# Kernel tuning notes

Measured on AMD Instinct MI355X. Metric: run time of the kernel, lower is better.

Reference implementation:

```python
import math
import jax, jax.numpy as jnp
import numpy as np

N_GAUSS = 1_000_000
EPS = 1e-8


def setup_inputs() -> dict:
    key = jax.random.key(0)
    k1, k2, k3 = jax.random.split(key, 3)
    init_extent = 50.0
    means = (jax.random.uniform(k1, (N_GAUSS, 3), dtype=jnp.float32) - 0.5) * 2.0 * init_extent
    log_scales = jnp.full((N_GAUSS, 3), math.log(0.05), dtype=jnp.float32)
    quats = jax.random.normal(k2, (N_GAUSS, 4), dtype=jnp.float32)
    sh_coeffs = jax.random.normal(k3, (N_GAUSS, 16, 3), dtype=jnp.float32) * 0.01
    opa_logit = math.log(0.1 / 0.9)  # inverse_sigmoid(init_opacity=0.1)
    opacity_camera = jnp.full((N_GAUSS, 1), opa_logit, dtype=jnp.float32)
    opacity_lidar = jnp.full((N_GAUSS, 1), opa_logit, dtype=jnp.float32)
    camera_to_world = jnp.eye(4, dtype=jnp.float32)
    lidar_to_world = jnp.eye(4, dtype=jnp.float32)
    intrinsics = jnp.array([[1000.0, 0.0, 800.0], [0.0, 1000.0, 450.0], [0.0, 0.0, 1.0]], dtype=jnp.float32)
    return dict(means=means, log_scales=log_scales, quats=quats, sh_coeffs=sh_coeffs,
                opacity_camera=opacity_camera, opacity_lidar=opacity_lidar,
                camera_to_world=camera_to_world, intrinsics=intrinsics,
                lidar_to_world=lidar_to_world,
                rgb_width=1600, rgb_height=900, lidar_width=1024, lidar_height=128,
                fov_min_deg=-25, fov_max_deg=3, near_plane=1, far_plane=100)


def _bilinear_scatter(u, v, w, vals, H, W, wrap_u):
    """Scatter vals [N,C] with weights w [N] at continuous pixel coords (u,v)
    using bilinear splatting. Returns [H, W, C+1] (weighted vals, weight sum)."""
    u0 = jnp.floor(u)
    v0 = jnp.floor(v)
    fu = u - u0
    fv = v - v0
    u0i = u0.astype(jnp.int32)
    v0i = v0.astype(jnp.int32)
    acc = jnp.zeros((H * W, vals.shape[-1] + 1), dtype=vals.dtype)
    corners = ((0, 0, (1.0 - fu) * (1.0 - fv)), (1, 0, fu * (1.0 - fv)),
               (0, 1, (1.0 - fu) * fv), (1, 1, fu * fv))
    for du, dv, cw in corners:
        ui = u0i + du
        vi = v0i + dv
        if wrap_u:
            ui = jnp.mod(ui, W)
            ok_u = jnp.ones_like(ui, dtype=bool)
        else:
            ok_u = (ui >= 0) & (ui < W)
        ok = ok_u & (vi >= 0) & (vi < H)
        ww = w * cw * ok.astype(w.dtype)
        idx = jnp.clip(vi, 0, H - 1) * W + jnp.clip(ui, 0, W - 1)
        payload = jnp.concatenate([vals * ww[:, None], ww[:, None]], axis=-1)
        acc = acc.at[idx].add(payload)
    return acc.reshape(H, W, -1)


def reference(means, log_scales, quats, sh_coeffs, opacity_camera, opacity_lidar,
              camera_to_world, intrinsics, lidar_to_world,
              rgb_width, rgb_height, lidar_width, lidar_height,
              fov_min_deg, fov_max_deg, near_plane, far_plane):
    H, W = int(rgb_height), int(rgb_width)
    HL, WL = int(lidar_height), int(lidar_width)
    near = float(near_plane)
    far = float(far_plane)

    # ---- camera (point-splat proxy of gsplat rasterization) ----
    w2c = jnp.linalg.inv(camera_to_world)
    pts_c = means @ w2c[:3, :3].T + w2c[:3, 3]  # [N,3] camera frame
    x, y, z = pts_c[:, 0], pts_c[:, 1], pts_c[:, 2]
    valid_c = (z > near) & (z < far)
    zs = jnp.where(valid_c, z, 1.0)
    u = intrinsics[0, 0] * x / zs + intrinsics[0, 2]
    v = intrinsics[1, 1] * y / zs + intrinsics[1, 2]
    opa_c = jax.nn.sigmoid(jnp.clip(opacity_camera[:, 0], -20.0, 20.0))
    colors = jax.nn.sigmoid(sh_coeffs[:, 0, :])  # DC band, as in render_rgb
    wc = opa_c * valid_c.astype(opa_c.dtype)
    vals_c = jnp.concatenate([colors, z[:, None]], axis=-1)  # [N,4] (rgb, depth)
    acc = _bilinear_scatter(u, v, wc, vals_c, H, W, wrap_u=False)
    wsum = acc[..., 4]
    alpha = jnp.clip(wsum, 0.0, 1.0)
    rgb = acc[..., :3] / (wsum[..., None] + EPS) * alpha[..., None]  # black background
    depth = acc[..., 3] / (wsum + EPS)

    # ---- LiDAR (custom spherical bilinear range-image splat, mean aggregation) ----
    w2l = jnp.linalg.inv(lidar_to_world)
    pts_l = means @ w2l[:3, :3].T + w2l[:3, 3]
    r = jnp.linalg.norm(pts_l, axis=-1)
    az = jnp.arctan2(pts_l[:, 1], pts_l[:, 0])
    el = jnp.arcsin(pts_l[:, 2] / jnp.maximum(r, 1e-6))
    fmin = math.radians(float(fov_min_deg))
    fmax = math.radians(float(fov_max_deg))
    uL = (az / (2.0 * jnp.pi) + 0.5) * WL          # azimuth wraps around
    vL = (fmax - el) / (fmax - fmin) * (HL - 1)    # elevation row
    valid_l = (r > near) & (r < far) & (el >= fmin) & (el <= fmax)
    opa_l = jax.nn.sigmoid(jnp.clip(opacity_lidar[:, 0], -20.0, 20.0))
    wl = opa_l * valid_l.astype(opa_l.dtype)
    acc_l = _bilinear_scatter(uL, vL, wl, r[:, None], HL, WL, wrap_u=True)
    lw = acc_l[..., 1]
    lidar_depth = acc_l[..., 0] / (lw + EPS)  # 'mean' depth aggregation
    lidar_alpha = jnp.clip(lw, 0.0, 1.0)

    return (rgb, depth, alpha, lidar_depth, lidar_alpha)
```

## Files before the change

kernel.cpp:

```cpp
#include <hip/hip_runtime.h>
#include <math.h>

#define EPSV 1e-8f
#define PI_D 3.14159265358979323846
#define NREP 8

__device__ float g_mats[32];

__device__ __forceinline__ void invert4x4_reg(const float* __restrict__ m,
                                              float* __restrict__ out) {
    double a00=m[0], a01=m[1], a02=m[2], a03=m[3];
    double a10=m[4], a11=m[5], a12=m[6], a13=m[7];
    double a20=m[8], a21=m[9], a22=m[10],a23=m[11];
    double a30=m[12],a31=m[13],a32=m[14],a33=m[15];

    double b00 = a00*a11 - a01*a10;
    double b01 = a00*a12 - a02*a10;
    double b02 = a00*a13 - a03*a10;
    double b03 = a01*a12 - a02*a11;
    double b04 = a01*a13 - a03*a11;
    double b05 = a02*a13 - a03*a12;
    double b06 = a20*a31 - a21*a30;
    double b07 = a20*a32 - a22*a30;
    double b08 = a20*a33 - a23*a30;
    double b09 = a21*a32 - a22*a31;
    double b10 = a21*a33 - a23*a31;
    double b11 = a22*a33 - a23*a32;

    double det = b00*b11 - b01*b10 + b02*b09 + b03*b08 - b04*b07 + b05*b06;
    double inv = 1.0 / det;

    out[0]  = (float)(( a11*b11 - a12*b10 + a13*b09) * inv);
    out[1]  = (float)((-a01*b11 + a02*b10 - a03*b09) * inv);
    out[2]  = (float)(( a31*b05 - a32*b04 + a33*b03) * inv);
    out[3]  = (float)((-a21*b05 + a22*b04 - a23*b03) * inv);
    out[4]  = (float)((-a10*b11 + a12*b08 - a13*b07) * inv);
    out[5]  = (float)(( a00*b11 - a02*b08 + a03*b07) * inv);
    out[6]  = (float)((-a30*b05 + a32*b02 - a33*b01) * inv);
    out[7]  = (float)(( a20*b05 - a22*b02 + a23*b01) * inv);
    out[8]  = (float)(( a10*b10 - a11*b08 + a13*b06) * inv);
    out[9]  = (float)((-a00*b10 + a01*b08 - a03*b06) * inv);
    out[10] = (float)(( a30*b04 - a31*b02 + a33*b00) * inv);
    out[11] = (float)((-a20*b04 + a21*b02 - a23*b00) * inv);
    out[12] = (float)((-a10*b09 + a11*b07 - a12*b06) * inv);
    out[13] = (float)(( a00*b09 - a01*b07 + a02*b06) * inv);
    out[14] = (float)((-a30*b03 + a31*b01 - a32*b00) * inv);
    out[15] = (float)(( a20*b03 - a21*b01 + a22*b00) * inv);
}

__global__ void prep_kernel(const float* __restrict__ c2w,
                            const float* __restrict__ l2w) {
    if (blockIdx.x == 0 && threadIdx.x == 0) {
        invert4x4_reg(c2w, g_mats);
        invert4x4_reg(l2w, g_mats + 16);
    }
}

__device__ __forceinline__ float sigmoid_clipped(float x) {
    #pragma clang fp contract(off)
    x = fminf(fmaxf(x, -20.0f), 20.0f);
    return 1.0f / (1.0f + expf(-x));
}

__global__ __launch_bounds__(256) void scatter_cam(
    const float* __restrict__ means,
    const float* __restrict__ sh,
    const float* __restrict__ opa_c,
    const float* __restrict__ intr,
    float* __restrict__ acc,
    const int* __restrict__ p_W, const int* __restrict__ p_H,
    const int* __restrict__ p_near, const int* __restrict__ p_far,
    int N)
{
    #pragma clang fp contract(off)
    const int t = blockIdx.x * blockDim.x + threadIdx.x;
    if (t >= N) return;

    const int W = *p_W, H = *p_H;
    const float nearp = (float)(*p_near);
    const float farp  = (float)(*p_far);
    const long long HW = (long long)W * H;

    float* C  = acc;
    float* Wp = acc + 4 * HW;

    const float fx = intr[0], cx = intr[2], fy = intr[4], cy = intr[5];
    const float* w2c = g_mats;

    const float px = means[3 * t + 0];
    const float py = means[3 * t + 1];
    const float pz = means[3 * t + 2];

    float x = w2c[0] * px + w2c[1] * py + w2c[2]  * pz + w2c[3];
    float y = w2c[4] * px + w2c[5] * py + w2c[6]  * pz + w2c[7];
    float z = w2c[8] * px + w2c[9] * py + w2c[10] * pz + w2c[11];
    if (!(z > nearp && z < farp)) return;

    float u = fx * x / z + cx;
    float v = fy * y / z + cy;
    float wc = sigmoid_clipped(opa_c[t]);
    const float* shp = sh + 48LL * t;
    float c0 = 1.0f / (1.0f + expf(-shp[0]));
    float c1 = 1.0f / (1.0f + expf(-shp[1]));
    float c2 = 1.0f / (1.0f + expf(-shp[2]));

    float u0f = floorf(u), v0f = floorf(v);
    float fu = u - u0f, fv = v - v0f;
    int u0 = (int)u0f, v0 = (int)v0f;
    #pragma unroll
    for (int c = 0; c < 4; c++) {
        int du = c & 1, dv = c >> 1;
        int ui = u0 + du, vi = v0 + dv;
        if (ui >= 0 && ui < W && vi >= 0 && vi < H) {
            float cw = (du ? fu : 1.0f - fu) * (dv ? fv : 1.0f - fv);
            float ww = wc * cw;
            long long idx = (long long)vi * W + ui;
            float* g = C + idx * 4;
            atomicAdd(g + 0, c0 * ww);
            atomicAdd(g + 1, c1 * ww);
            atomicAdd(g + 2, c2 * ww);
            atomicAdd(g + 3, z * ww);
            atomicAdd(Wp + idx, ww);
        }
    }
}

__global__ __launch_bounds__(256) void scatter_lid(
    const float* __restrict__ means,
    const float* __restrict__ opa_l,
    float* __restrict__ acc,
    const int* __restrict__ p_W, const int* __restrict__ p_H,
    const int* __restrict__ p_WL, const int* __restrict__ p_HL,
    const int* __restrict__ p_fmin, const int* __restrict__ p_fmax,
    const int* __restrict__ p_near, const int* __restrict__ p_far,
    int N)
{
    #pragma clang fp contract(off)
    const int t = blockIdx.x * blockDim.x + threadIdx.x;
    if (t >= N) return;

    const int W = *p_W, H = *p_H, WL = *p_WL, HL = *p_HL;
    const float nearp = (float)(*p_near);
    const float farp  = (float)(*p_far);
    const double dfmin = (double)(*p_fmin) * PI_D / 180.0;
    const double dfmax = (double)(*p_fmax) * PI_D / 180.0;
    const float ffmin  = (float)dfmin;
    const float ffmax  = (float)dfmax;
    const float denomL = (float)(dfmax - dfmin);
    const float twopi  = (float)(2.0 * PI_D);

    const long long HW  = (long long)W * H;
    const long long LHW = (long long)WL * HL;

    float* Lr = acc + 5 * HW + (long long)(blockIdx.x & (NREP - 1)) * 2 * LHW;

    const float* w2l = g_mats + 16;

    const float px = means[3 * t + 0];
    const float py = means[3 * t + 1];
    const float pz = means[3 * t + 2];

    float x = w2l[0] * px + w2l[1] * py + w2l[2]  * pz + w2l[3];
    float y = w2l[4] * px + w2l[5] * py + w2l[6]  * pz + w2l[7];
    float z = w2l[8] * px + w2l[9] * py + w2l[10] * pz + w2l[11];
    float rr = ((x * x) + (y * y)) + (z * z);
    float r = sqrtf(rr);
    float q  = z / fmaxf(r, 1e-6f);
    float el = (float)asin((double)q);
    if (!(r > nearp && r < farp && el >= ffmin && el <= ffmax)) return;

    float az = (float)atan2((double)y, (double)x);
    float uL = (az / twopi + 0.5f) * (float)WL;
    float vL = (ffmax - el) / denomL * (float)(HL - 1);
    float wl = sigmoid_clipped(opa_l[t]);

    float u0f = floorf(uL), v0f = floorf(vL);
    float fu = uL - u0f, fv = vL - v0f;
    int u0 = (int)u0f, v0 = (int)v0f;
    #pragma unroll
    for (int c = 0; c < 4; c++) {
        int du = c & 1, dv = c >> 1;
        int ui = u0 + du, vi = v0 + dv;
        if (ui >= WL) ui -= WL;
        if (vi >= 0 && vi < HL) {
            float cw = (du ? fu : 1.0f - fu) * (dv ? fv : 1.0f - fv);
            float ww = wl * cw;
            long long idx = (long long)vi * WL + ui;
            atomicAdd(Lr + 2 * idx + 0, r * ww);
            atomicAdd(Lr + 2 * idx + 1, ww);
        }
    }
}

__global__ __launch_bounds__(256) void finalize_acc(
    const float* __restrict__ acc,
    float* __restrict__ out,
    const int* __restrict__ p_W, const int* __restrict__ p_H,
    const int* __restrict__ p_WL, const int* __restrict__ p_HL)
{
    const int W = *p_W, H = *p_H, WL = *p_WL, HL = *p_HL;
    const long long HW = (long long)W * H;
    const long long LHW = (long long)WL * HL;
    const long long depthOff = 3 * HW;
    const long long alphaOff = 4 * HW;
    const long long ldOff    = 5 * HW;
    const long long laOff    = 5 * HW + LHW;

    const float* C  = acc;
    const float* Wp = acc + 4 * HW;
    const float* L  = acc + 5 * HW;

    long long i = (long long)blockIdx.x * blockDim.x + threadIdx.x;
    if (i < HW) {
        float4 p = *reinterpret_cast<const float4*>(C + 4 * i);
        float wsum = Wp[i];
        float a = fminf(fmaxf(wsum, 0.0f), 1.0f);
        float inv = 1.0f / (wsum + EPSV);
        float s = inv * a;
        out[3 * i + 0] = p.x * s;
        out[3 * i + 1] = p.y * s;
        out[3 * i + 2] = p.z * s;
        out[depthOff + i] = p.w * inv;
        out[alphaOff + i] = a;
    }
    if (i < LHW) {
        float ld = 0.0f, lw = 0.0f;
        #pragma unroll
        for (int k = 0; k < NREP; k++) {
            float2 l = *reinterpret_cast<const float2*>(L + (long long)k * 2 * LHW + 2 * i);
            ld += l.x;
            lw += l.y;
        }
        out[ldOff + i] = ld * (1.0f / (lw + EPSV));
        out[laOff + i] = fminf(fmaxf(lw, 0.0f), 1.0f);
    }
}

__global__ __launch_bounds__(256) void scatter_fb(
    const float* __restrict__ means,
    const float* __restrict__ sh,
    const float* __restrict__ opa_c,
    const float* __restrict__ opa_l,
    const float* __restrict__ intr,
    const int* __restrict__ p_W, const int* __restrict__ p_H,
    const int* __restrict__ p_WL, const int* __restrict__ p_HL,
    const int* __restrict__ p_fmin, const int* __restrict__ p_fmax,
    const int* __restrict__ p_near, const int* __restrict__ p_far,
    float* __restrict__ out, int N)
{
    #pragma clang fp contract(off)
    const int t = blockIdx.x * blockDim.x + threadIdx.x;
    if (t >= N) return;

    const int W = *p_W, H = *p_H, WL = *p_WL, HL = *p_HL;
    const float nearp = (float)(*p_near);
    const float farp  = (float)(*p_far);
    const double dfmin = (double)(*p_fmin) * PI_D / 180.0;
    const double dfmax = (double)(*p_fmax) * PI_D / 180.0;
    const float ffmin  = (float)dfmin;
    const float ffmax  = (float)dfmax;
    const float denomL = (float)(dfmax - dfmin);
    const float twopi  = (float)(2.0 * PI_D);

    const long long HW = (long long)W * H;
    const long long LHW = (long long)WL * HL;
    const long long depthOff = 3 * HW;
    const long long alphaOff = 4 * HW;
    const long long ldOff    = 5 * HW;
    const long long laOff    = 5 * HW + LHW;

    const float fx = intr[0], cx = intr[2], fy = intr[4], cy = intr[5];
    const float* w2c = g_mats;
    const float* w2l = g_mats + 16;

    const float px = means[3 * t + 0];
    const float py = means[3 * t + 1];
    const float pz = means[3 * t + 2];
    {
        float x = w2c[0] * px + w2c[1] * py + w2c[2]  * pz + w2c[3];
        float y = w2c[4] * px + w2c[5] * py + w2c[6]  * pz + w2c[7];
        float z = w2c[8] * px + w2c[9] * py + w2c[10] * pz + w2c[11];
        if (z > nearp && z < farp) {
            float u = fx * x / z + cx;
            float v = fy * y / z + cy;
            float wc = sigmoid_clipped(opa_c[t]);
            const float* shp = sh + 48LL * t;
            float c0 = 1.0f / (1.0f + expf(-shp[0]));
            float c1 = 1.0f / (1.0f + expf(-shp[1]));
            float c2 = 1.0f / (1.0f + expf(-shp[2]));

            float u0f = floorf(u), v0f = floorf(v);
            float fu = u - u0f, fv = v - v0f;
            int u0 = (int)u0f, v0 = (int)v0f;
            #pragma unroll
            for (int c = 0; c < 4; c++) {
                int du = c & 1, dv = c >> 1;
                int ui = u0 + du, vi = v0 + dv;
                if (ui >= 0 && ui < W && vi >= 0 && vi < H) {
                    float cw = (du ? fu : 1.0f - fu) * (dv ? fv : 1.0f - fv);
                    float ww = wc * cw;
                    long long idx = (long long)vi * W + ui;
                    atomicAdd(&out[idx * 3 + 0], c0 * ww);
                    atomicAdd(&out[idx * 3 + 1], c1 * ww);
                    atomicAdd(&out[idx * 3 + 2], c2 * ww);
                    atomicAdd(&out[depthOff + idx], z * ww);
                    atomicAdd(&out[alphaOff + idx], ww);
                }
            }
        }
    }
    {
        float x = w2l[0] * px + w2l[1] * py + w2l[2]  * pz + w2l[3];
        float y = w2l[4] * px + w2l[5] * py + w2l[6]  * pz + w2l[7];
        float z = w2l[8] * px + w2l[9] * py + w2l[10] * pz + w2l[11];
        float rr = ((x * x) + (y * y)) + (z * z);
        float r = sqrtf(rr);
        float q  = z / fmaxf(r, 1e-6f);
        float el = (float)asin((double)q);
        if (r > nearp && r < farp && el >= ffmin && el <= ffmax) {
            float az = (float)atan2((double)y, (double)x);
            float uL = (az / twopi + 0.5f) * (float)WL;
            float vL = (ffmax - el) / denomL * (float)(HL - 1);
            float wl = sigmoid_clipped(opa_l[t]);

            float u0f = floorf(uL), v0f = floorf(vL);
            float fu = uL - u0f, fv = vL - v0f;
            int u0 = (int)u0f, v0 = (int)v0f;
            #pragma unroll
            for (int c = 0; c < 4; c++) {
                int du = c & 1, dv = c >> 1;
                int ui = u0 + du, vi = v0 + dv;
                if (ui >= WL) ui -= WL;
                if (vi >= 0 && vi < HL) {
                    float cw = (du ? fu : 1.0f - fu) * (dv ? fv : 1.0f - fv);
                    float ww = wl * cw;
                    long long idx = (long long)vi * WL + ui;
                    atomicAdd(&out[ldOff + idx], r * ww);
                    atomicAdd(&out[laOff + idx], ww);
                }
            }
        }
    }
}

__global__ __launch_bounds__(256) void finalize_fb(
    float* __restrict__ out,
    const int* __restrict__ p_W, const int* __restrict__ p_H,
    const int* __restrict__ p_WL, const int* __restrict__ p_HL)
{
    const int W = *p_W, H = *p_H, WL = *p_WL, HL = *p_HL;
    const long long HW = (long long)W * H;
    const long long LHW = (long long)WL * HL;
    const long long depthOff = 3 * HW;
    const long long alphaOff = 4 * HW;
    const long long ldOff    = 5 * HW;
    const long long laOff    = 5 * HW + LHW;

    long long i = (long long)blockIdx.x * blockDim.x + threadIdx.x;
    if (i < HW) {
        float wsum = out[alphaOff + i];
        float a = fminf(fmaxf(wsum, 0.0f), 1.0f);
        float inv = 1.0f / (wsum + EPSV);
        float s = inv * a;
        out[3 * i + 0] *= s;
        out[3 * i + 1] *= s;
        out[3 * i + 2] *= s;
        out[depthOff + i] *= inv;
        out[alphaOff + i] = a;
    }
    if (i < LHW) {
        float wsum = out[laOff + i];
        out[ldOff + i] *= 1.0f / (wsum + EPSV);
        out[laOff + i] = fminf(fmaxf(wsum, 0.0f), 1.0f);
    }
}

extern "C" void kernel_launch(void* const* d_in, const int* in_sizes, int n_in,
                              void* d_out, int out_size, void* d_ws, size_t ws_size,
                              hipStream_t stream) {
    const float* means  = (const float*)d_in[0];
    const float* sh     = (const float*)d_in[3];
    const float* opa_c  = (const float*)d_in[4];
    const float* opa_l  = (const float*)d_in[5];
    const float* c2w    = (const float*)d_in[6];
    const float* intr   = (const float*)d_in[7];
    const float* l2w    = (const float*)d_in[8];
    const int* p_W    = (const int*)d_in[9];
    const int* p_H    = (const int*)d_in[10];
    const int* p_WL   = (const int*)d_in[11];
    const int* p_HL   = (const int*)d_in[12];
    const int* p_fmin = (const int*)d_in[13];
    const int* p_fmax = (const int*)d_in[14];
    const int* p_near = (const int*)d_in[15];
    const int* p_far  = (const int*)d_in[16];

    const int N = in_sizes[0] / 3;
    float* out = (float*)d_out;
    float* acc = (float*)d_ws;

    const long long HW  = 1600LL * 900LL;
    const long long LHW = 1024LL * 128LL;
    const size_t need_bytes =
        (5 * (size_t)HW + (size_t)NREP * 2 * (size_t)LHW) * sizeof(float);

    const int sgrid = (N + 255) / 256;
    const int fgrid = (int)((HW + 255) / 256);

    prep_kernel<<<1, 64, 0, stream>>>(c2w, l2w);

    if (ws_size >= need_bytes) {
        hipMemsetAsync(d_ws, 0, need_bytes, stream);
        scatter_cam<<<sgrid, 256, 0, stream>>>(
            means, sh, opa_c, intr, acc,
            p_W, p_H, p_near, p_far, N);
        scatter_lid<<<sgrid, 256, 0, stream>>>(
            means, opa_l, acc,
            p_W, p_H, p_WL, p_HL, p_fmin, p_fmax, p_near, p_far, N);
        finalize_acc<<<fgrid, 256, 0, stream>>>(
            acc, out, p_W, p_H, p_WL, p_HL);
    } else {
        hipMemsetAsync(d_out, 0, (size_t)out_size * sizeof(float), stream);
        scatter_fb<<<sgrid, 256, 0, stream>>>(
            means, sh, opa_c, opa_l, intr,
            p_W, p_H, p_WL, p_HL, p_fmin, p_fmax, p_near, p_far,
            out, N);
        finalize_fb<<<fgrid, 256, 0, stream>>>(
            out, p_W, p_H, p_WL, p_HL);
    }
}
```

Measured before the change: 426.3 us.

## Fuse camera and lidar scatters with packed 64-bit CAS accumulation

Merges the camera and lidar scatter kernels into one kernel and drops the separate matrix-inversion kernel. Each block now inverts the 4x4 matrices into shared memory. Pairs of float accumulators are packed into 64-bit words and updated with a compare-and-swap loop, which cuts the number of atomic operations per corner. The cost is possible CAS retry loops under contention, since many Gaussians hit the same pixels, plus redundant per-block matrix inversion in double precision.

```diff
diff --git a/kernel.cpp b/kernel.cpp
--- a/kernel.cpp
+++ b/kernel.cpp
@@ -5,7 +5,7 @@
 #define PI_D 3.14159265358979323846
 #define NREP 8
 
-__device__ float g_mats[32];
+typedef unsigned long long ull_t;
 
 __device__ __forceinline__ void invert4x4_reg(const float* __restrict__ m,
                                               float* __restrict__ out) {
@@ -48,86 +48,35 @@
     out[15] = (float)(( a20*b03 - a21*b01 + a22*b00) * inv);
 }
 
-__global__ void prep_kernel(const float* __restrict__ c2w,
-                            const float* __restrict__ l2w) {
-    if (blockIdx.x == 0 && threadIdx.x == 0) {
-        invert4x4_reg(c2w, g_mats);
-        invert4x4_reg(l2w, g_mats + 16);
-    }
-}
-
 __device__ __forceinline__ float sigmoid_clipped(float x) {
     #pragma clang fp contract(off)
     x = fminf(fmaxf(x, -20.0f), 20.0f);
     return 1.0f / (1.0f + expf(-x));
 }
 
-__global__ __launch_bounds__(256) void scatter_cam(
+__device__ __forceinline__ ull_t pack2(float a, float b) {
+    return ((ull_t)__float_as_uint(b) << 32) | (ull_t)__float_as_uint(a);
+}
+__device__ __forceinline__ void cas_add2(ull_t* p, float da, float db) {
+    ull_t old = *p;
+    while (true) {
+        float a = __uint_as_float((unsigned int)(old & 0xffffffffULL));
+        float b = __uint_as_float((unsigned int)(old >> 32));
+        ull_t desired = pack2(a + da, b + db);
+        ull_t got = atomicCAS(p, old, desired);
+        if (got == old) break;
+        old = got;
+    }
+}
+
+__global__ __launch_bounds__(256) void scatter_pk(
     const float* __restrict__ means,
     const float* __restrict__ sh,
     const float* __restrict__ opa_c,
+    const float* __restrict__ opa_l,
     const float* __restrict__ intr,
-    float* __restrict__ acc,
-    const int* __restrict__ p_W, const int* __restrict__ p_H,
-    const int* __restrict__ p_near, const int* __restrict__ p_far,
-    int N)
-{
-    #pragma clang fp contract(off)
-    const int t = blockIdx.x * blockDim.x + threadIdx.x;
-    if (t >= N) return;
-
-    const int W = *p_W, H = *p_H;
-    const float nearp = (float)(*p_near);
-    const float farp  = (float)(*p_far);
-    const long long HW = (long long)W * H;
-
-    float* C  = acc;
-    float* Wp = acc + 4 * HW;
-
-    const float fx = intr[0], cx = intr[2], fy = intr[4], cy = intr[5];
-    const float* w2c = g_mats;
-
-    const float px = means[3 * t + 0];
-    const float py = means[3 * t + 1];
-    const float pz = means[3 * t + 2];
-
-    float x = w2c[0] * px + w2c[1] * py + w2c[2]  * pz + w2c[3];
-    float y = w2c[4] * px + w2c[5] * py + w2c[6]  * pz + w2c[7];
-    float z = w2c[8] * px + w2c[9] * py + w2c[10] * pz + w2c[11];
-    if (!(z > nearp && z < farp)) return;
-
-    float u = fx * x / z + cx;
-    float v = fy * y / z + cy;
-    float wc = sigmoid_clipped(opa_c[t]);
-    const float* shp = sh + 48LL * t;
-    float c0 = 1.0f / (1.0f + expf(-shp[0]));
-    float c1 = 1.0f / (1.0f + expf(-shp[1]));
-    float c2 = 1.0f / (1.0f + expf(-shp[2]));
-
-    float u0f = floorf(u), v0f = floorf(v);
-    float fu = u - u0f, fv = v - v0f;
-    int u0 = (int)u0f, v0 = (int)v0f;
-    #pragma unroll
-    for (int c = 0; c < 4; c++) {
-        int du = c & 1, dv = c >> 1;
-        int ui = u0 + du, vi = v0 + dv;
-        if (ui >= 0 && ui < W && vi >= 0 && vi < H) {
-            float cw = (du ? fu : 1.0f - fu) * (dv ? fv : 1.0f - fv);
-            float ww = wc * cw;
-            long long idx = (long long)vi * W + ui;
-            float* g = C + idx * 4;
-            atomicAdd(g + 0, c0 * ww);
-            atomicAdd(g + 1, c1 * ww);
-            atomicAdd(g + 2, c2 * ww);
-            atomicAdd(g + 3, z * ww);
-            atomicAdd(Wp + idx, ww);
-        }
-    }
-}
-
-__global__ __launch_bounds__(256) void scatter_lid(
-    const float* __restrict__ means,
-    const float* __restrict__ opa_l,
+    const float* __restrict__ c2w,
+    const float* __restrict__ l2w,
     float* __restrict__ acc,
     const int* __restrict__ p_W, const int* __restrict__ p_H,
     const int* __restrict__ p_WL, const int* __restrict__ p_HL,
@@ -136,6 +85,13 @@
     int N)
 {
     #pragma clang fp contract(off)
+    __shared__ float sm[32];
+    if (threadIdx.x == 0) {
+        invert4x4_reg(c2w, sm);
+        invert4x4_reg(l2w, sm + 16);
+    }
+    __syncthreads();
+
     const int t = blockIdx.x * blockDim.x + threadIdx.x;
     if (t >= N) return;
 
@@ -152,47 +108,85 @@
     const long long HW  = (long long)W * H;
     const long long LHW = (long long)WL * HL;
 
-    float* Lr = acc + 5 * HW + (long long)(blockIdx.x & (NREP - 1)) * 2 * LHW;
-
-    const float* w2l = g_mats + 16;
+    ull_t* C01 = (ull_t*)acc;
+    ull_t* C23 = (ull_t*)(acc + 2 * HW);
+    float* Wp  = acc + 4 * HW;
+    ull_t* Lr  = (ull_t*)(acc + 5 * HW) + (long long)(blockIdx.x & (NREP - 1)) * LHW;
+
+    const float fx = intr[0], cx = intr[2], fy = intr[4], cy = intr[5];
+    const float* w2c = sm;
+    const float* w2l = sm + 16;
 
     const float px = means[3 * t + 0];
     const float py = means[3 * t + 1];
     const float pz = means[3 * t + 2];
 
-    float x = w2l[0] * px + w2l[1] * py + w2l[2]  * pz + w2l[3];
-    float y = w2l[4] * px + w2l[5] * py + w2l[6]  * pz + w2l[7];
-    float z = w2l[8] * px + w2l[9] * py + w2l[10] * pz + w2l[11];
-    float rr = ((x * x) + (y * y)) + (z * z);
-    float r = sqrtf(rr);
-    float q  = z / fmaxf(r, 1e-6f);
-    float el = (float)asin((double)q);
-    if (!(r > nearp && r < farp && el >= ffmin && el <= ffmax)) return;
-
-    float az = (float)atan2((double)y, (double)x);
-    float uL = (az / twopi + 0.5f) * (float)WL;
-    float vL = (ffmax - el) / denomL * (float)(HL - 1);
-    float wl = sigmoid_clipped(opa_l[t]);
-
-    float u0f = floorf(uL), v0f = floorf(vL);
-    float fu = uL - u0f, fv = vL - v0f;
-    int u0 = (int)u0f, v0 = (int)v0f;
-    #pragma unroll
-    for (int c = 0; c < 4; c++) {
-        int du = c & 1, dv = c >> 1;
-        int ui = u0 + du, vi = v0 + dv;
-        if (ui >= WL) ui -= WL;
-        if (vi >= 0 && vi < HL) {
-            float cw = (du ? fu : 1.0f - fu) * (dv ? fv : 1.0f - fv);
-            float ww = wl * cw;
-            long long idx = (long long)vi * WL + ui;
-            atomicAdd(Lr + 2 * idx + 0, r * ww);
-            atomicAdd(Lr + 2 * idx + 1, ww);
+    {
+        float x = w2c[0] * px + w2c[1] * py + w2c[2]  * pz + w2c[3];
+        float y = w2c[4] * px + w2c[5] * py + w2c[6]  * pz + w2c[7];
+        float z = w2c[8] * px + w2c[9] * py + w2c[10] * pz + w2c[11];
+        if (z > nearp && z < farp) {
+            float u = fx * x / z + cx;
+            float v = fy * y / z + cy;
+            float wc = sigmoid_clipped(opa_c[t]);
+            const float* shp = sh + 48LL * t;
+            float c0 = 1.0f / (1.0f + expf(-shp[0]));
+            float c1 = 1.0f / (1.0f + expf(-shp[1]));
+            float c2 = 1.0f / (1.0f + expf(-shp[2]));
+
+            float u0f = floorf(u), v0f = floorf(v);
+            float fu = u - u0f, fv = v - v0f;
+            int u0 = (int)u0f, v0 = (int)v0f;
+            #pragma unroll
+            for (int c = 0; c < 4; c++) {
+                int du = c & 1, dv = c >> 1;
+                int ui = u0 + du, vi = v0 + dv;
+                if (ui >= 0 && ui < W && vi >= 0 && vi < H) {
+                    float cw = (du ? fu : 1.0f - fu) * (dv ? fv : 1.0f - fv);
+                    float ww = wc * cw;
+                    long long idx = (long long)vi * W + ui;
+                    cas_add2(C01 + idx, c0 * ww, c1 * ww);
+                    cas_add2(C23 + idx, c2 * ww, z * ww);
+                    atomicAdd(Wp + idx, ww);
+                }
+            }
         }
     }
-}
-
-__global__ __launch_bounds__(256) void finalize_acc(
+
+    {
+        float x = w2l[0] * px + w2l[1] * py + w2l[2]  * pz + w2l[3];
+        float y = w2l[4] * px + w2l[5] * py + w2l[6]  * pz + w2l[7];
+        float z = w2l[8] * px + w2l[9] * py + w2l[10] * pz + w2l[11];
+        float rr = ((x * x) + (y * y)) + (z * z);
+        float r = sqrtf(rr);
+        float q  = z / fmaxf(r, 1e-6f);
+        float el = (float)asin((double)q);
+        if (r > nearp && r < farp && el >= ffmin && el <= ffmax) {
+            float az = (float)atan2((double)y, (double)x);
+            float uL = (az / twopi + 0.5f) * (float)WL;
+            float vL = (ffmax - el) / denomL * (float)(HL - 1);
+            float wl = sigmoid_clipped(opa_l[t]);
+
+            float u0f = floorf(uL), v0f = floorf(vL);
+            float fu = uL - u0f, fv = vL - v0f;
+            int u0 = (int)u0f, v0 = (int)v0f;
+            #pragma unroll
+            for (int c = 0; c < 4; c++) {
+                int du = c & 1, dv = c >> 1;
+                int ui = u0 + du, vi = v0 + dv;
+                if (ui >= WL) ui -= WL;
+                if (vi >= 0 && vi < HL) {
+                    float cw = (du ? fu : 1.0f - fu) * (dv ? fv : 1.0f - fv);
+                    float ww = wl * cw;
+                    long long idx = (long long)vi * WL + ui;
+                    cas_add2(Lr + idx, r * ww, ww);
+                }
+            }
+        }
+    }
+}
+
+__global__ __launch_bounds__(256) void finalize_pk(
     const float* __restrict__ acc,
     float* __restrict__ out,
     const int* __restrict__ p_W, const int* __restrict__ p_H,
@@ -206,30 +200,35 @@
     const long long ldOff    = 5 * HW;
     const long long laOff    = 5 * HW + LHW;
 
-    const float* C  = acc;
-    const float* Wp = acc + 4 * HW;
-    const float* L  = acc + 5 * HW;
+    const ull_t* C01 = (const ull_t*)acc;
+    const ull_t* C23 = (const ull_t*)(acc + 2 * HW);
+    const float* Wp  = acc + 4 * HW;
+    const ull_t* L   = (const ull_t*)(acc + 5 * HW);
 
     long long i = (long long)blockIdx.x * blockDim.x + threadIdx.x;
     if (i < HW) {
-        float4 p = *reinterpret_cast<const float4*>(C + 4 * i);
+        ull_t v01 = C01[i], v23 = C23[i];
+        float c0 = __uint_as_float((unsigned int)(v01 & 0xffffffffULL));
+        float c1 = __uint_as_float((unsigned int)(v01 >> 32));
+        float c2 = __uint_as_float((unsigned int)(v23 & 0xffffffffULL));
+        float zz = __uint_as_float((unsigned int)(v23 >> 32));
         float wsum = Wp[i];
         float a = fminf(fmaxf(wsum, 0.0f), 1.0f);
         float inv = 1.0f / (wsum + EPSV);
         float s = inv * a;
-        out[3 * i + 0] = p.x * s;
-        out[3 * i + 1] = p.y * s;
-        out[3 * i + 2] = p.z * s;
-        out[depthOff + i] = p.w * inv;
+        out[3 * i + 0] = c0 * s;
+        out[3 * i + 1] = c1 * s;
+        out[3 * i + 2] = c2 * s;
+        out[depthOff + i] = zz * inv;
         out[alphaOff + i] = a;
     }
     if (i < LHW) {
         float ld = 0.0f, lw = 0.0f;
         #pragma unroll
         for (int k = 0; k < NREP; k++) {
-            float2 l = *reinterpret_cast<const float2*>(L + (long long)k * 2 * LHW + 2 * i);
-            ld += l.x;
-            lw += l.y;
+            ull_t v = L[(long long)k * LHW + i];
+            ld += __uint_as_float((unsigned int)(v & 0xffffffffULL));
+            lw += __uint_as_float((unsigned int)(v >> 32));
         }
         out[ldOff + i] = ld * (1.0f / (lw + EPSV));
         out[laOff + i] = fminf(fmaxf(lw, 0.0f), 1.0f);
@@ -242,6 +241,8 @@
     const float* __restrict__ opa_c,
     const float* __restrict__ opa_l,
     const float* __restrict__ intr,
+    const float* __restrict__ c2w,
+    const float* __restrict__ l2w,
     const int* __restrict__ p_W, const int* __restrict__ p_H,
     const int* __restrict__ p_WL, const int* __restrict__ p_HL,
     const int* __restrict__ p_fmin, const int* __restrict__ p_fmax,
@@ -249,6 +250,13 @@
     float* __restrict__ out, int N)
 {
     #pragma clang fp contract(off)
+    __shared__ float sm[32];
+    if (threadIdx.x == 0) {
+        invert4x4_reg(c2w, sm);
+        invert4x4_reg(l2w, sm + 16);
+    }
+    __syncthreads();
+
     const int t = blockIdx.x * blockDim.x + threadIdx.x;
     if (t >= N) return;
 
@@ -270,8 +278,8 @@
     const long long laOff    = 5 * HW + LHW;
 
     const float fx = intr[0], cx = intr[2], fy = intr[4], cy = intr[5];
-    const float* w2c = g_mats;
-    const float* w2l = g_mats + 16;
+    const float* w2c = sm;
+    const float* w2l = sm + 16;
 
     const float px = means[3 * t + 0];
     const float py = means[3 * t + 1];
@@ -406,22 +414,17 @@
     const int sgrid = (N + 255) / 256;
     const int fgrid = (int)((HW + 255) / 256);
 
-    prep_kernel<<<1, 64, 0, stream>>>(c2w, l2w);
-
     if (ws_size >= need_bytes) {
         hipMemsetAsync(d_ws, 0, need_bytes, stream);
-        scatter_cam<<<sgrid, 256, 0, stream>>>(
-            means, sh, opa_c, intr, acc,
-            p_W, p_H, p_near, p_far, N);
-        scatter_lid<<<sgrid, 256, 0, stream>>>(
-            means, opa_l, acc,
+        scatter_pk<<<sgrid, 256, 0, stream>>>(
+            means, sh, opa_c, opa_l, intr, c2w, l2w, acc,
             p_W, p_H, p_WL, p_HL, p_fmin, p_fmax, p_near, p_far, N);
-        finalize_acc<<<fgrid, 256, 0, stream>>>(
+        finalize_pk<<<fgrid, 256, 0, stream>>>(
             acc, out, p_W, p_H, p_WL, p_HL);
     } else {
         hipMemsetAsync(d_out, 0, (size_t)out_size * sizeof(float), stream);
         scatter_fb<<<sgrid, 256, 0, stream>>>(
-            means, sh, opa_c, opa_l, intr,
+            means, sh, opa_c, opa_l, intr, c2w, l2w,
             p_W, p_H, p_WL, p_HL, p_fmin, p_fmax, p_near, p_far,
             out, N);
         finalize_fb<<<fgrid, 256, 0, stream>>>(
```

Measured after the change: 384.2 us. -9.9%, faster.
